# Performance work log

Hardware: AMD Instinct MI355X
Metric: run time of the kernel (lower is better)

## Reference

```python
import jax, jax.numpy as jnp
import numpy as np

NUM_HEADS = 16
NUM_KV_HEADS = 4
HEAD_DIM = 256
ROPE_THETA = 10000.0


def _rope(x, position_ids):
    # x: [B, H, S, D], position_ids: [B, S]
    d = x.shape[-1]
    inv_freq = 1.0 / (ROPE_THETA ** (jnp.arange(0, d, 2, dtype=jnp.float32) / d))  # [D/2]
    freqs = position_ids.astype(jnp.float32)[:, :, None] * inv_freq[None, None, :]  # [B, S, D/2]
    emb = jnp.concatenate([freqs, freqs], axis=-1)  # [B, S, D]
    cos = jnp.cos(emb)[:, None, :, :]
    sin = jnp.sin(emb)[:, None, :, :]
    x1, x2 = jnp.split(x, 2, axis=-1)
    rot = jnp.concatenate([-x2, x1], axis=-1)
    return x * cos + rot * sin


def setup_inputs() -> dict:
    key = jax.random.key(0)
    k1, k2, k3, k4, k5 = jax.random.split(key, 5)
    B, S, H = 2, 2048, 2048
    hidden_states = jax.random.normal(k1, (B, S, H), dtype=jnp.float32)
    position_ids = jnp.broadcast_to(jnp.arange(S, dtype=jnp.int32)[None, :], (B, S))
    scale = 1.0 / np.sqrt(H)
    wq = jax.random.normal(k2, (H, NUM_HEADS * HEAD_DIM), dtype=jnp.float32) * scale
    wk = jax.random.normal(k3, (H, NUM_KV_HEADS * HEAD_DIM), dtype=jnp.float32) * scale
    wv = jax.random.normal(k4, (H, NUM_KV_HEADS * HEAD_DIM), dtype=jnp.float32) * scale
    wo = jax.random.normal(k5, (NUM_HEADS * HEAD_DIM, H), dtype=jnp.float32) * (1.0 / np.sqrt(NUM_HEADS * HEAD_DIM))
    return {"hidden_states": hidden_states, "position_ids": position_ids,
            "wq": wq, "wk": wk, "wv": wv, "wo": wo}


def reference(hidden_states, position_ids, wq, wk, wv, wo):
    B, S, H = hidden_states.shape
    groups = NUM_HEADS // NUM_KV_HEADS
    # QKV projections -> [B, heads, S, D]
    q = (hidden_states @ wq).reshape(B, S, NUM_HEADS, HEAD_DIM).transpose(0, 2, 1, 3)
    k = (hidden_states @ wk).reshape(B, S, NUM_KV_HEADS, HEAD_DIM).transpose(0, 2, 1, 3)
    v = (hidden_states @ wv).reshape(B, S, NUM_KV_HEADS, HEAD_DIM).transpose(0, 2, 1, 3)
    q = _rope(q, position_ids)
    k = _rope(k, position_ids)
    # GQA without materializing repeated K/V: group query heads per kv head
    qg = q.reshape(B, NUM_KV_HEADS, groups, S, HEAD_DIM)
    scale = 1.0 / jnp.sqrt(jnp.asarray(HEAD_DIM, dtype=q.dtype))
    scores = jnp.einsum('bkgqd,bkvd->bkgqv', qg, k) * scale  # [B, KV, G, S, S]
    causal = jnp.tril(jnp.ones((S, S), dtype=bool))
    scores = jnp.where(causal[None, None, None, :, :], scores, jnp.finfo(scores.dtype).min)
    probs = jax.nn.softmax(scores, axis=-1)
    out = jnp.einsum('bkgqv,bkvd->bkgqd', probs, v)  # [B, KV, G, S, D]
    out = out.reshape(B, NUM_HEADS, S, HEAD_DIM).transpose(0, 2, 1, 3).reshape(B, S, NUM_HEADS * HEAD_DIM)
    return out @ wo
```

## Files before the change

kernel.cpp:

```cpp
#include <hip/hip_runtime.h>

typedef unsigned short u16;
typedef __bf16 bf16_t;
typedef bf16_t bf16x8 __attribute__((ext_vector_type(8)));
typedef float f32x4 __attribute__((ext_vector_type(4)));
typedef float f32x16 __attribute__((ext_vector_type(16)));

#define LOG2E 1.4426950408889634f
#define QKVS 6144

__device__ __forceinline__ u16 f2bf(float f) {
  union { float f; unsigned u; } c; c.f = f;
  unsigned r = c.u + 0x7fffu + ((c.u >> 16) & 1u);
  return (u16)(r >> 16);
}
__device__ __forceinline__ float bf2f(u16 u) {
  union { unsigned u; float f; } c; c.u = ((unsigned)u) << 16;
  return c.f;
}

__device__ __forceinline__ void gload16(const void* g, void* l) {
  __builtin_amdgcn_global_load_lds(
      (const __attribute__((address_space(1))) unsigned int*)g,
      (__attribute__((address_space(3))) unsigned int*)l, 16, 0, 0);
}

__device__ __forceinline__ unsigned cvtpk(float lo, float hi) {
  unsigned r;
  asm("v_cvt_pk_bf16_f32 %0, %1, %2" : "=v"(r) : "v"(lo), "v"(hi));
  return r;
}
__device__ __forceinline__ void swap32(unsigned& a, unsigned& b) {
  asm("v_permlane32_swap_b32 %0, %1" : "+v"(a), "+v"(b));
}

#define MFMA16(a, b, c) __builtin_amdgcn_mfma_f32_16x16x32_bf16((a), (b), (c), 0, 0, 0)
#define MFMA32(a, b, c) __builtin_amdgcn_mfma_f32_32x32x16_bf16((a), (b), (c), 0, 0, 0)

__global__ __launch_bounds__(256) void k_prep(const float* __restrict__ hs,
                                              const int* __restrict__ pos,
                                              const float* __restrict__ wq,
                                              const float* __restrict__ wk,
                                              const float* __restrict__ wv,
                                              const float* __restrict__ wo,
                                              u16* __restrict__ Xb,
                                              u16* __restrict__ Wqkvt,
                                              u16* __restrict__ Wot,
                                              float2* __restrict__ tab) {
  __shared__ float tile[32][33];
  const int fb = blockIdx.x;
  if (fb < 8192) {
    int i = fb * 256 + threadIdx.x;
    float4 v = ((const float4*)hs)[i];
    ushort4 o;
    o.x = f2bf(v.x); o.y = f2bf(v.y); o.z = f2bf(v.z); o.w = f2bf(v.w);
    ((ushort4*)Xb)[i] = o;
    return;
  }
  if (fb >= 28672) {
    int idx = (fb - 28672) * 256 + threadIdx.x;
    int i = idx & 127, row = idx >> 7;
    float p = (float)pos[row];
    float f = p * exp2f((float)i * (-13.287712379549449f / 128.f));
    float sn, cs;
    sincosf(f, &sn, &cs);
    tab[idx] = make_float2(cs, sn);
    return;
  }
  const float* in;
  u16* out;
  int R, C, bxi, byi;
  if (fb < 16384) {
    in = wq; out = Wqkvt; R = 2048; C = 4096;
    int l = fb - 8192; bxi = l & 127; byi = l >> 7;
  } else if (fb < 18432) {
    in = wk; out = Wqkvt + 4096 * 2048; R = 2048; C = 1024;
    int l = fb - 16384; bxi = l & 31; byi = l >> 5;
  } else if (fb < 20480) {
    in = wv; out = Wqkvt + 5120 * 2048; R = 2048; C = 1024;
    int l = fb - 18432; bxi = l & 31; byi = l >> 5;
  } else {
    in = wo; out = Wot; R = 4096; C = 2048;
    int l = fb - 20480; bxi = l & 63; byi = l >> 6;
  }
  int tx = threadIdx.x & 31, ty = threadIdx.x >> 5;
  int bx = bxi * 32, by = byi * 32;
#pragma unroll
  for (int i = 0; i < 4; i++)
    tile[ty + i * 8][tx] = in[(size_t)(by + ty + i * 8) * C + bx + tx];
  __syncthreads();
#pragma unroll
  for (int i = 0; i < 4; i++)
    out[(size_t)(bx + ty + i * 8) * R + by + tx] = f2bf(tile[tx][ty + i * 8]);
}


template <int OUT_BF16>
__global__ __launch_bounds__(256) void k_gemm_bt(const u16* __restrict__ A,
                                                 const u16* __restrict__ Bt,
                                                 void* __restrict__ C, int M, int N, int K) {
  __shared__ u16 As[128 * 64];
  __shared__ u16 Bs[128 * 64];
  const int tid = threadIdx.x;
  const int lane = tid & 63;
  const int w = tid >> 6;
  const int l15 = lane & 15, l4 = lane >> 4;
  const int wr = w >> 1, wc = w & 1;
  const int bx = blockIdx.x, by = blockIdx.y;

  f32x4 acc[4][4];
#pragma unroll
  for (int a = 0; a < 4; a++)
#pragma unroll
    for (int b2 = 0; b2 < 4; b2++) acc[a][b2] = (f32x4){0.f, 0.f, 0.f, 0.f};

  const u16* Abase = A + (size_t)by * 128 * K;
  const u16* Bbase = Bt + (size_t)bx * 128 * K;

  for (int kk = 0; kk < K; kk += 64) {
    __syncthreads();
#pragma unroll
    for (int j = 0; j < 4; j++) {
      int ci = w * 256 + j * 64 + lane;
      int row = ci >> 3, c = ci & 7;
      gload16(Abase + (size_t)row * K + kk + c * 8, (char*)As + ci * 16);
      gload16(Bbase + (size_t)row * K + kk + c * 8, (char*)Bs + ci * 16);
    }
    __syncthreads();
#pragma unroll
    for (int kc = 0; kc < 2; kc++) {
      int kb = kc * 64 + l4 * 16;
      bf16x8 av[4], bv[4];
#pragma unroll
      for (int mt = 0; mt < 4; mt++)
        av[mt] = *(const bf16x8*)((const char*)As + (wr * 64 + mt * 16 + l15) * 128 + kb);
#pragma unroll
      for (int nt = 0; nt < 4; nt++)
        bv[nt] = *(const bf16x8*)((const char*)Bs + (wc * 64 + nt * 16 + l15) * 128 + kb);
#pragma unroll
      for (int mt = 0; mt < 4; mt++)
#pragma unroll
        for (int nt = 0; nt < 4; nt++) acc[mt][nt] = MFMA16(av[mt], bv[nt], acc[mt][nt]);
    }
  }
#pragma unroll
  for (int mt = 0; mt < 4; mt++) {
#pragma unroll
    for (int nt = 0; nt < 4; nt++) {
      int col = bx * 128 + wc * 64 + nt * 16 + l15;
#pragma unroll
      for (int r = 0; r < 4; r++) {
        int row = by * 128 + wr * 64 + mt * 16 + l4 * 4 + r;
        if (OUT_BF16)
          ((u16*)C)[(size_t)row * N + col] = f2bf(acc[mt][nt][r]);
        else
          ((float*)C)[(size_t)row * N + col] = acc[mt][nt][r];
      }
    }
  }
}


__global__ __launch_bounds__(512, 1) void k_gemm256(const u16* __restrict__ A,
                                                    const u16* __restrict__ Bt,
                                                    u16* __restrict__ C, int N, int K,
                                                    const float2* __restrict__ tab,
                                                    u16* __restrict__ Vt) {
  extern __shared__ char smem[];
  const int tid = threadIdx.x;
  const int lane = tid & 63, w = tid >> 6;
  const int l15 = lane & 15, l4 = lane >> 4;
  const int wr = w >> 2, wc = w & 3;
  const int bx = blockIdx.x, by = blockIdx.y;
  const int NT = K >> 6;

  const u16* Ab = A + (size_t)(by * 256) * K;
  const u16* Bb = Bt + (size_t)(bx * 256) * K;

  int srcoff[2], dstoff[2];
#pragma unroll
  for (int rr = 0; rr < 2; rr++) {
    int ci = rr * 512 + tid;
    int lc = ci ^ (((ci >> 5) & 1) << 1);
    int kc = lc >> 9, row = (lc >> 2) & 127, g2 = lc & 3;
    srcoff[rr] = row * K + kc * 32 + g2 * 8;
    dstoff[rr] = ci * 16;
  }

  auto SH = [&](int Tg, int halfidx) {
    const u16* base = (halfidx < 2) ? (Ab + (size_t)(halfidx * 128) * K)
                                    : (Bb + (size_t)((halfidx - 2) * 128) * K);
    char* dst = smem + (Tg & 1) * 65536 + halfidx * 16384;
    int kk = Tg * 64;
#pragma unroll
    for (int rr = 0; rr < 2; rr++)
      gload16(base + srcoff[rr] + kk, dst + dstoff[rr]);
  };

  auto lda = [&](int c, int kc, int mrow4) -> bf16x8 {
    int L = kc * 8192 + (mrow4 * 16 + l15) * 64 + l4 * 16;
    int P = L ^ (((L >> 9) & 1) << 5);
    return *(const bf16x8*)(smem + c * 65536 + wr * 16384 + P);
  };
  auto ldb = [&](int c, int kc, int j) -> bf16x8 {
    int L = kc * 8192 + ((wc & 1) * 64 + j * 16 + l15) * 64 + l4 * 16;
    int P = L ^ (((L >> 9) & 1) << 5);
    return *(const bf16x8*)(smem + c * 65536 + 32768 + (wc >> 1) * 16384 + P);
  };

  f32x4 acc[8][4];
#pragma unroll
  for (int i = 0; i < 8; i++)
#pragma unroll
    for (int j = 0; j < 4; j++) acc[i][j] = (f32x4){0.f, 0.f, 0.f, 0.f};

  SH(0, 0); SH(0, 1); SH(0, 2); SH(0, 3);
  SH(1, 2); SH(1, 3);
  asm volatile("s_waitcnt vmcnt(4)" ::: "memory");
  __builtin_amdgcn_s_barrier();
  asm volatile("" ::: "memory");

  bf16x8 bv[2][4];
  for (int T = 0; T < NT; ++T) {
    const int c = T & 1;
#pragma unroll
    for (int q = 0; q < 4; q++) {
      const int kc = q & 1, mh = q >> 1;
      bf16x8 av[4];
      if (q < 2) {
#pragma unroll
        for (int j = 0; j < 4; j++) bv[kc][j] = ldb(c, kc, j);
      }
#pragma unroll
      for (int ii = 0; ii < 4; ii++) av[ii] = lda(c, kc, mh * 4 + ii);
      if (q == 0)      { if (T + 1 < NT) SH(T + 1, 0); }
      else if (q == 1) { if (T + 1 < NT) SH(T + 1, 1); }
      else if (q == 2) { if (T + 2 < NT) SH(T + 2, 2); }
      else             { if (T + 2 < NT) SH(T + 2, 3); }
      if (q == 3) {
        if (T < NT - 2)       asm volatile("s_waitcnt vmcnt(4)" ::: "memory");
        else if (T == NT - 2) asm volatile("s_waitcnt vmcnt(0)" ::: "memory");
      }
      asm volatile("" ::: "memory");
      __builtin_amdgcn_s_barrier();
      asm volatile("" ::: "memory");
      asm volatile("s_waitcnt lgkmcnt(0)" ::: "memory");
      __builtin_amdgcn_sched_barrier(0);
      __builtin_amdgcn_s_setprio(1);
#pragma unroll
      for (int ii = 0; ii < 4; ii++)
#pragma unroll
        for (int j = 0; j < 4; j++)
          acc[mh * 4 + ii][j] = MFMA16(av[ii], bv[kc][j], acc[mh * 4 + ii][j]);
      __builtin_amdgcn_s_setprio(0);
      asm volatile("" ::: "memory");
      __builtin_amdgcn_s_barrier();
      asm volatile("" ::: "memory");
    }
  }

  if (bx < 20) {
    float4* X4 = (float4*)smem;
    const float sgn = (wc < 2) ? -1.f : 1.f;
    const int ptid = tid ^ 128;
#pragma unroll
    for (int ih = 0; ih < 2; ih++) {
      __syncthreads();
#pragma unroll
      for (int i2 = 0; i2 < 4; i2++)
#pragma unroll
        for (int j2 = 0; j2 < 4; j2++) {
          f32x4 a = acc[ih * 4 + i2][j2];
          X4[(i2 * 4 + j2) * 512 + tid] = make_float4(a[0], a[1], a[2], a[3]);
        }
      __syncthreads();
#pragma unroll
      for (int i2 = 0; i2 < 4; i2++) {
#pragma unroll
        for (int j2 = 0; j2 < 4; j2++) {
          int col = bx * 256 + wc * 64 + j2 * 16 + l15;
          int ti = (wc & 1) * 64 + j2 * 16 + l15;
          float4 part = X4[(i2 * 4 + j2) * 512 + ptid];
          float pa[4] = {part.x, part.y, part.z, part.w};
#pragma unroll
          for (int r2 = 0; r2 < 4; r2++) {
            int row = by * 256 + wr * 128 + (ih * 4 + i2) * 16 + l4 * 4 + r2;
            float mine = acc[ih * 4 + i2][j2][r2];
            float2 t = tab[(size_t)row * 128 + ti];
            C[(size_t)row * N + col] = f2bf(mine * t.x + sgn * pa[r2] * t.y);
          }
        }
      }
    }
  } else {
    u16* lt = (u16*)smem;
    const int vbase = bx * 256 - 5120;
#pragma unroll
    for (int ih = 0; ih < 2; ih++) {
      __syncthreads();
#pragma unroll
      for (int i2 = 0; i2 < 4; i2++) {
#pragma unroll
        for (int j2 = 0; j2 < 4; j2++) {
          int col = wc * 64 + j2 * 16 + l15;
          int lrow = wr * 64 + i2 * 16 + l4 * 4;
          f32x4 a = acc[ih * 4 + i2][j2];
          ushort4 pk;
          pk.x = f2bf(a[0]); pk.y = f2bf(a[1]); pk.z = f2bf(a[2]); pk.w = f2bf(a[3]);
          *(ushort4*)&lt[col * 136 + lrow] = pk;
        }
      }
      __syncthreads();
#pragma unroll
      for (int v = 0; v < 8; v++) {
        int idx2 = v * 512 + tid;
        int vc = idx2 >> 4, tv = idx2 & 15;
        bf16x8 val = *(const bf16x8*)&lt[vc * 136 + tv * 8];
        int token = by * 256 + ((tv < 8) ? (ih * 64 + tv * 8) : (128 + ih * 64 + (tv - 8) * 8));
        *(bf16x8*)&Vt[(size_t)(vbase + vc) * 4096 + token] = val;
      }
    }
  }
}


__shared__ __align__(16) u16 aK0[8192];
__shared__ __align__(16) u16 aK1[8192];
__shared__ __align__(16) u16 aV0[8192];
__shared__ __align__(16) u16 aV1[8192];

__global__ __launch_bounds__(256, 2) void k_attn(const u16* __restrict__ QKV,
                                                 const u16* __restrict__ Vt,
                                                 u16* __restrict__ AO) {
  const int tid = threadIdx.x, lane = tid & 63, w = tid >> 6;
  const int r31 = lane & 31, hi = lane >> 5;

  const int flat = blockIdx.x;
  const int r = flat & 7;
  const int idx = flat >> 3;
  const int b = r >> 2, kv = r & 3;
  const int half = idx >> 5, j = idx & 31;
  const int qb = half ? 15 - (j >> 1) : (j >> 1);
  const int h = kv * 4 + (j & 1) + 2 * half;

  bf16x8 qreg[16];
  {
    const u16* qp = QKV + (size_t)(b * 2048 + qb * 128 + w * 32 + r31) * QKVS + h * 256 + hi * 8;
#pragma unroll
    for (int kc = 0; kc < 16; kc++) qreg[kc] = *(const bf16x8*)(qp + kc * 16);
  }

  f32x16 o[8];
#pragma unroll
  for (int df = 0; df < 8; df++)
#pragma unroll
    for (int jj = 0; jj < 16; jj++) o[df][jj] = 0.f;
  float mrow = -3e38f, lrow = 0.f;

  const int nt = 4 * qb + 4;
  const int tlim = 4 * qb + w;
  const int qloc = qb * 128 + w * 32 + r31;
  const u16* Kbase = QKV + (size_t)(b * 2048) * QKVS + 4096 + kv * 256;
  const u16* Vbase = Vt + (size_t)(kv * 256) * 4096 + b * 2048;

  int kfix[4], vfix[4];
#pragma unroll
  for (int jj = 0; jj < 4; jj++) {
    int ci = jj * 256 + tid;
    int krow = ci >> 5, kc = ci & 31;
    int kcg = (kc & 24) | ((kc ^ krow) & 7);
    kfix[jj] = krow * QKVS + kcg * 8;
    int vrow = ci >> 2, vc = ci & 3;
    int vg = (vc - (vrow >> 1)) & 3;
    vfix[jj] = vrow * 4096 + vg * 8;
  }
  int koff = 0, voff = 0;

  auto STAGE = [&](u16* Kd, u16* Vd) {
#pragma unroll
    for (int jj = 0; jj < 4; jj++)
      gload16(Kbase + kfix[jj] + koff, (char*)Kd + (jj * 256 + tid) * 16);
#pragma unroll
    for (int jj = 0; jj < 4; jj++)
      gload16(Vbase + vfix[jj] + voff, (char*)Vd + (jj * 256 + tid) * 16);
    koff += 32 * QKVS;
    voff += 32;
  };

  auto COMPUTE = [&](int t, const u16* Kc, const u16* Vc) {
    f32x16 s;
#pragma unroll
    for (int jj = 0; jj < 16; jj++) s[jj] = 0.f;
#pragma unroll
    for (int kc = 0; kc < 16; kc++) {
      int ch = kc * 2 + hi;
      int cs = (ch & 24) | ((ch ^ r31) & 7);
      bf16x8 kf = *(const bf16x8*)((const char*)Kc + r31 * 512 + cs * 16);
      s = MFMA32(kf, qreg[kc], s);
    }

    const float C = 0.0625f * LOG2E;
    float z[16];
#pragma unroll
    for (int jj = 0; jj < 16; jj++) z[jj] = s[jj] * C;
    if (t == tlim) {
#pragma unroll
      for (int jj = 0; jj < 16; jj++) {
        int kvg = t * 32 + (jj & 3) + 8 * (jj >> 2) + 4 * hi;
        if (kvg > qloc) z[jj] = -1e30f;
      }
    }

    float m0 = z[0];
#pragma unroll
    for (int jj = 1; jj < 16; jj++) m0 = fmaxf(m0, z[jj]);
    m0 = fmaxf(m0, __shfl_xor(m0, 32));
    if (__any(m0 > mrow + 11.54f)) {
      float mn = fmaxf(mrow, m0);
      float alpha = exp2f(mrow - mn);
      mrow = mn;
      lrow *= alpha;
#pragma unroll
      for (int jj = 0; jj < 16; jj++) {
        float a = __shfl(alpha, (jj & 3) + 8 * (jj >> 2) + 4 * hi);
#pragma unroll
        for (int df = 0; df < 8; df++) o[df][jj] *= a;
      }
    }
    float sum = 0.f;
#pragma unroll
    for (int jj = 0; jj < 16; jj++) {
      z[jj] = exp2f(z[jj] - mrow);
      sum += z[jj];
    }
    sum += __shfl_xor(sum, 32);
    lrow += sum;

    unsigned a0 = cvtpk(z[0], z[1]), a2 = cvtpk(z[4], z[5]);
    swap32(a0, a2);
    unsigned a1 = cvtpk(z[2], z[3]), a3 = cvtpk(z[6], z[7]);
    swap32(a1, a3);
    unsigned b0 = cvtpk(z[8], z[9]), b2 = cvtpk(z[12], z[13]);
    swap32(b0, b2);
    unsigned b1 = cvtpk(z[10], z[11]), b3 = cvtpk(z[14], z[15]);
    swap32(b1, b3);
    union UU { unsigned u[4]; bf16x8 v; };
    UU ua; ua.u[0] = a0; ua.u[1] = a1; ua.u[2] = a2; ua.u[3] = a3;
    UU ub; ub.u[0] = b0; ub.u[1] = b1; ub.u[2] = b2; ub.u[3] = b3;
    bf16x8 pa0 = ua.v, pa1 = ub.v;

#pragma unroll
    for (int df = 0; df < 8; df++) {
      int vr = df * 32 + r31;
      int c0 = (hi + (vr >> 1)) & 3;
      int c1 = (2 + hi + (vr >> 1)) & 3;
      bf16x8 v0 = *(const bf16x8*)((const char*)Vc + vr * 64 + c0 * 16);
      bf16x8 v1 = *(const bf16x8*)((const char*)Vc + vr * 64 + c1 * 16);
      o[df] = MFMA32(pa0, v0, o[df]);
      o[df] = MFMA32(pa1, v1, o[df]);
    }
  };

  STAGE(aK0, aV0);
  __syncthreads();

  for (int t = 0; t < nt; t += 2) {
    STAGE(aK1, aV1);
    if (t <= tlim) COMPUTE(t, aK0, aV0);
    __syncthreads();
    if (t + 2 < nt) STAGE(aK0, aV0);
    if (t + 1 <= tlim) COMPUTE(t + 1, aK1, aV1);
    __syncthreads();
  }

  float rl = 1.f / lrow;
  size_t rowbase = (size_t)(b * 2048 + qb * 128 + w * 32);
#pragma unroll
  for (int jj = 0; jj < 16; jj++) {
    float rr2 = __shfl(rl, (jj & 3) + 8 * (jj >> 2) + 4 * hi);
    int qr = (jj & 3) + 8 * (jj >> 2) + 4 * hi;
#pragma unroll
    for (int df = 0; df < 8; df++)
      AO[(rowbase + qr) * 4096 + h * 256 + df * 32 + r31] = f2bf(o[df][jj] * rr2);
  }
}


#define OFF_AO    0u
#define OFF_XB    0u
#define OFF_WQKVT 16777216u
#define OFF_WOT   41943040u
#define OFF_QKV   58720256u
#define OFF_TAB   109051904u
#define OFF_VT    113246208u

extern "C" void kernel_launch(void* const* d_in, const int* in_sizes, int n_in,
                              void* d_out, int out_size, void* d_ws, size_t ws_size,
                              hipStream_t stream) {
  const float* hs = (const float*)d_in[0];
  const int* pos = (const int*)d_in[1];
  const float* wq = (const float*)d_in[2];
  const float* wk = (const float*)d_in[3];
  const float* wv = (const float*)d_in[4];
  const float* wo = (const float*)d_in[5];
  float* out = (float*)d_out;
  char* ws = (char*)d_ws;

  u16* Xb    = (u16*)(ws + OFF_XB);
  u16* Wqkvt = (u16*)(ws + OFF_WQKVT);
  u16* Wot   = (u16*)(ws + OFF_WOT);
  u16* QKV   = (u16*)(ws + OFF_QKV);
  float2* Tab = (float2*)(ws + OFF_TAB);
  u16* Vt    = (u16*)(ws + OFF_VT);
  u16* AO    = (u16*)(ws + OFF_AO);

  k_prep<<<30720, 256, 0, stream>>>(hs, pos, wq, wk, wv, wo, Xb, Wqkvt, Wot, Tab);

  (void)hipFuncSetAttribute((const void*)k_gemm256,
                            hipFuncAttributeMaxDynamicSharedMemorySize, 131072);
  k_gemm256<<<dim3(24, 16), 512, 131072, stream>>>(Xb, Wqkvt, QKV, 6144, 2048, Tab, Vt);

  k_attn<<<dim3(512), 256, 0, stream>>>(QKV, Vt, AO);

  k_gemm_bt<0><<<dim3(16, 32), 256, 0, stream>>>(AO, Wot, out, 4096, 2048, 4096);
}
```

Before: 453.8 us.

## Split attention KV range into two halves with a separate merge kernel

Each query block's causal KV range is now split across two workgroups (split-KV, flash-decoding style), doubling the attention grid to 1024 blocks. Each half writes a normalized partial output (one to AO, one to the output buffer used as scratch) plus its row max and sum, and a new merge kernel combines them with log-sum-exp weights. The aim is better load balance and occupancy for the triangular workload. The cost is an extra kernel launch, additional global traffic for the partials, and a second bf16 rounding of the outputs.

```diff
diff --git a/kernel.cpp b/kernel.cpp
--- a/kernel.cpp
+++ b/kernel.cpp
@@ -331,7 +331,9 @@
 
 __global__ __launch_bounds__(256, 2) void k_attn(const u16* __restrict__ QKV,
                                                  const u16* __restrict__ Vt,
-                                                 u16* __restrict__ AO) {
+                                                 u16* __restrict__ AO,
+                                                 u16* __restrict__ Pd,
+                                                 float2* __restrict__ ML) {
   const int tid = threadIdx.x, lane = tid & 63, w = tid >> 6;
   const int r31 = lane & 31, hi = lane >> 5;
 
@@ -339,9 +341,10 @@
   const int r = flat & 7;
   const int idx = flat >> 3;
   const int b = r >> 2, kv = r & 3;
-  const int half = idx >> 5, j = idx & 31;
-  const int qb = half ? 15 - (j >> 1) : (j >> 1);
-  const int h = kv * 4 + (j & 1) + 2 * half;
+  const int g = idx & 1;
+  const int e = idx >> 1;
+  const int qb = 15 - (e >> 2);
+  const int h = kv * 4 + (e & 3);
 
   bf16x8 qreg[16];
   {
@@ -357,7 +360,8 @@
     for (int jj = 0; jj < 16; jj++) o[df][jj] = 0.f;
   float mrow = -3e38f, lrow = 0.f;
 
-  const int nt = 4 * qb + 4;
+  const int hh = 2 * qb + 2;
+  const int t0 = g * hh;
   const int tlim = 4 * qb + w;
   const int qloc = qb * 128 + w * 32 + r31;
   const u16* Kbase = QKV + (size_t)(b * 2048) * QKVS + 4096 + kv * 256;
@@ -374,7 +378,7 @@
     int vg = (vc - (vrow >> 1)) & 3;
     vfix[jj] = vrow * 4096 + vg * 8;
   }
-  int koff = 0, voff = 0;
+  int koff = t0 * 32 * QKVS, voff = t0 * 32;
 
   auto STAGE = [&](u16* Kd, u16* Vd) {
 #pragma unroll
@@ -464,16 +468,18 @@
   STAGE(aK0, aV0);
   __syncthreads();
 
-  for (int t = 0; t < nt; t += 2) {
+  for (int tt = 0; tt < hh; tt += 2) {
+    int t = t0 + tt;
     STAGE(aK1, aV1);
     if (t <= tlim) COMPUTE(t, aK0, aV0);
     __syncthreads();
-    if (t + 2 < nt) STAGE(aK0, aV0);
+    if (tt + 2 < hh) STAGE(aK0, aV0);
     if (t + 1 <= tlim) COMPUTE(t + 1, aK1, aV1);
     __syncthreads();
   }
 
-  float rl = 1.f / lrow;
+  float rl = (lrow > 0.f) ? 1.f / lrow : 0.f;
+  u16* dst = g ? Pd : AO;
   size_t rowbase = (size_t)(b * 2048 + qb * 128 + w * 32);
 #pragma unroll
   for (int jj = 0; jj < 16; jj++) {
@@ -481,14 +487,40 @@
     int qr = (jj & 3) + 8 * (jj >> 2) + 4 * hi;
 #pragma unroll
     for (int df = 0; df < 8; df++)
-      AO[(rowbase + qr) * 4096 + h * 256 + df * 32 + r31] = f2bf(o[df][jj] * rr2);
-  }
+      dst[(rowbase + qr) * 4096 + h * 256 + df * 32 + r31] = f2bf(o[df][jj] * rr2);
+  }
+  if (hi == 0) {
+    int token = b * 2048 + qloc;
+    ML[g * 65536 + token * 16 + h] = make_float2(mrow, lrow);
+  }
+}
+
+__global__ __launch_bounds__(256) void k_merge(u16* __restrict__ AO,
+                                               const u16* __restrict__ Pd,
+                                               const float2* __restrict__ ML) {
+  int idx = blockIdx.x * 256 + threadIdx.x;
+  int rh = idx >> 5, dblk = idx & 31;
+  float2 ml0 = ML[rh], ml1 = ML[65536 + rh];
+  float mm = fmaxf(ml0.x, ml1.x);
+  float w0 = ml0.y * exp2f(ml0.x - mm);
+  float w1 = ml1.y * exp2f(ml1.x - mm);
+  float rs = 1.f / (w0 + w1);
+  size_t off = (size_t)rh * 256 + dblk * 8;
+  union BU { bf16x8 v; u16 a[8]; };
+  BU a, bb, o;
+  a.v = *(const bf16x8*)(AO + off);
+  bb.v = *(const bf16x8*)(Pd + off);
+#pragma unroll
+  for (int e = 0; e < 8; e++)
+    o.a[e] = f2bf((bf2f(a.a[e]) * w0 + bf2f(bb.a[e]) * w1) * rs);
+  *(bf16x8*)(AO + off) = o.v;
 }
 
 
 #define OFF_AO    0u
 #define OFF_XB    0u
 #define OFF_WQKVT 16777216u
+#define OFF_ML    33554432u
 #define OFF_WOT   41943040u
 #define OFF_QKV   58720256u
 #define OFF_TAB   109051904u
@@ -508,11 +540,13 @@
 
   u16* Xb    = (u16*)(ws + OFF_XB);
   u16* Wqkvt = (u16*)(ws + OFF_WQKVT);
+  float2* ML = (float2*)(ws + OFF_ML);
   u16* Wot   = (u16*)(ws + OFF_WOT);
   u16* QKV   = (u16*)(ws + OFF_QKV);
   float2* Tab = (float2*)(ws + OFF_TAB);
   u16* Vt    = (u16*)(ws + OFF_VT);
   u16* AO    = (u16*)(ws + OFF_AO);
+  u16* Pd    = (u16*)d_out;
 
   k_prep<<<30720, 256, 0, stream>>>(hs, pos, wq, wk, wv, wo, Xb, Wqkvt, Wot, Tab);
 
@@ -520,7 +554,9 @@
                             hipFuncAttributeMaxDynamicSharedMemorySize, 131072);
   k_gemm256<<<dim3(24, 16), 512, 131072, stream>>>(Xb, Wqkvt, QKV, 6144, 2048, Tab, Vt);
 
-  k_attn<<<dim3(512), 256, 0, stream>>>(QKV, Vt, AO);
+  k_attn<<<dim3(1024), 256, 0, stream>>>(QKV, Vt, AO, Pd, ML);
+
+  k_merge<<<8192, 256, 0, stream>>>(AO, Pd, ML);
 
   k_gemm_bt<0><<<dim3(16, 32), 256, 0, stream>>>(AO, Wot, out, 4096, 2048, 4096);
 }
```

Result: faster. 444.0 us (median of 2 runs) (-2.2%).
